# Optimization experiments

Measured on AMD Instinct MI355X. Metric: run time of the kernel, lower is better.

The kernel has to match this reference:

```python
import jax, jax.numpy as jnp
import numpy as np

DIM = 1024
HEADS = 16

def setup_inputs() -> dict:
    key = jax.random.key(0)
    k1, k2, k3, k4 = jax.random.split(key, 4)
    x = jax.random.normal(k1, (2, 2048, DIM), dtype=jnp.float32)
    # torch Linear weights are [out_features, in_features]
    w_qkv = jax.random.normal(k2, (3 * DIM, DIM), dtype=jnp.float32) * (DIM ** -0.5)
    w_out = jax.random.normal(k3, (DIM, DIM), dtype=jnp.float32) * (DIM ** -0.5)
    b_out = jax.random.normal(k4, (DIM,), dtype=jnp.float32) * 0.01
    return {"x": x, "w_qkv": w_qkv, "w_out": w_out, "b_out": b_out}

def reference(x, w_qkv, w_out, b_out):
    b, n, dim = x.shape
    h = HEADS
    d = dim // h
    scale = dim ** -0.5  # NOTE: full dim, faithful to source
    qkv = x @ w_qkv.T                       # [b, n, 3*dim]
    qkv = qkv.reshape(b, n, 3, h, d)        # split (qkv h d)
    q, k, v = (qkv[:, :, i].transpose(0, 2, 1, 3) for i in range(3))  # [b, h, n, d]
    scores = jnp.einsum('bhid,bhjd->bhij', q, k) * scale
    weights = jax.nn.softmax(scores, axis=-1)
    out = jnp.einsum('bhij,bhjd->bhid', weights, v)  # [b, h, n, d]
    out = out.transpose(0, 2, 1, 3).reshape(b, n, dim)
    return out @ w_out.T + b_out
```

## Files before the change

kernel.cpp:

```cpp
#include <hip/hip_runtime.h>

#define DIM   1024
#define HEADS 16
#define NSEQ  2048
#define BATCH 2

typedef unsigned short u16;
typedef unsigned long long u64;
typedef __attribute__((ext_vector_type(8))) short bf16x8;
typedef __attribute__((ext_vector_type(4))) float f32x4;
typedef __attribute__((ext_vector_type(16))) float f32x16;

__device__ __forceinline__ u16 f2b(float f) {
  union { float f; unsigned u; } v; v.f = f;
  unsigned r = (v.u + 0x7fffu + ((v.u >> 16) & 1u)) >> 16;
  return (u16)r;
}

__device__ __forceinline__ void g2l16(const u16* g, u16* l) {
  __builtin_amdgcn_global_load_lds(
      (const __attribute__((address_space(1))) void*)g,
      (__attribute__((address_space(3))) void*)l, 16, 0, 0);
}

__global__ void cvt_bf16(const float* __restrict__ src, u16* __restrict__ dst,
                         int n4, int sc4, float s) {
  int i = blockIdx.x * blockDim.x + threadIdx.x;
  if (i < n4) {
    float4 f = ((const float4*)src)[i];
    float m = (i < sc4) ? s : 1.0f;
    union { u16 s[4]; u64 ll; } o;
    o.s[0] = f2b(f.x * m); o.s[1] = f2b(f.y * m);
    o.s[2] = f2b(f.z * m); o.s[3] = f2b(f.w * m);
    ((u64*)dst)[i] = o.ll;
  }
}

__global__ __launch_bounds__(256, 2)
void gemm_bt(const u16* __restrict__ A, const u16* __restrict__ Bt,
             void* __restrict__ C, const float* __restrict__ bias,
             int M, int Nc, int K, int bf16_out) {
  __shared__ u16 As[128 * 64];
  __shared__ u16 Bs[128 * 64];
  const int tid  = threadIdx.x;
  const int wave = tid >> 6, lane = tid & 63;
  const int l15  = lane & 15, quad = lane >> 4;
  const int m0 = blockIdx.y * 128, n0 = blockIdx.x * 128;
  const int wm = (wave >> 1) * 64, wn = (wave & 1) * 64;
  const int rb = wave * 32;

  f32x4 acc[4][4] = {};

  for (int kt = 0; kt < K; kt += 64) {
#pragma unroll
    for (int c = 0; c < 4; ++c) {
      int r  = rb + c * 8 + (lane >> 3);
      int ck = (lane & 7) ^ (r & 7);
      g2l16(A  + (size_t)(m0 + r) * K + kt + ck * 8, &As[(rb + c * 8) * 64]);
      g2l16(Bt + (size_t)(n0 + r) * K + kt + ck * 8, &Bs[(rb + c * 8) * 64]);
    }
    __syncthreads();
#pragma unroll
    for (int ks = 0; ks < 2; ++ks) {
      bf16x8 a[4], b[4];
      int ch = ks * 4 + quad;
#pragma unroll
      for (int i = 0; i < 4; ++i) {
        int ra  = wm + i * 16 + l15;
        a[i] = *(const bf16x8*)&As[ra * 64 + ((ch ^ (ra & 7)) << 3)];
        int rb2 = wn + i * 16 + l15;
        b[i] = *(const bf16x8*)&Bs[rb2 * 64 + ((ch ^ (rb2 & 7)) << 3)];
      }
#pragma unroll
      for (int i = 0; i < 4; ++i)
#pragma unroll
        for (int j = 0; j < 4; ++j)
          acc[i][j] = __builtin_amdgcn_mfma_f32_16x16x32_bf16(a[i], b[j], acc[i][j], 0, 0, 0);
    }
    __syncthreads();
  }

#pragma unroll
  for (int i = 0; i < 4; ++i)
#pragma unroll
    for (int j = 0; j < 4; ++j) {
      int row = m0 + wm + i * 16 + quad * 4;
      int col = n0 + wn + j * 16 + l15;
#pragma unroll
      for (int r = 0; r < 4; ++r) {
        float v = acc[i][j][r];
        if (bf16_out) ((u16*)C)[(size_t)(row + r) * Nc + col] = f2b(v);
        else          ((float*)C)[(size_t)(row + r) * Nc + col] = v + bias[col];
      }
    }
}

__global__ __launch_bounds__(256, 1)
void attn(const u16* __restrict__ qkv, u16* __restrict__ outp) {
  __shared__ u16 Ks[2][128 * 64];
  __shared__ u16 Vts[2][64 * 128];
  const int tid  = threadIdx.x;
  const int wave = tid >> 6, lane = tid & 63;
  const int l31  = lane & 31, h = lane >> 5;
  const int b = blockIdx.x >> 4, hd = blockIdx.x & 15;
  const int q0 = blockIdx.y * 256;
  const u16* base = qkv + (size_t)b * NSEQ * 3072;
  const int qoff = hd * 64, koff = DIM + hd * 64, voff = 2 * DIM + hd * 64;
  const int dc = tid & 7, j0l = (tid >> 3) * 4;
  const int vchunk = (j0l >> 4) * 2 + ((j0l >> 2) & 1);
  const int vboff  = 4 * ((j0l >> 3) & 1);

  union V4 { uint4 q; u16 s[8]; };
  union PA { unsigned w[4]; bf16x8 f; };

#pragma unroll
  for (int c = 0; c < 8; ++c) {
    int bse = wave * 64 + c * 8;
    g2l16(base + (size_t)(q0 + bse + (lane >> 3)) * 3072 + qoff + (((lane & 7) ^ ((lane >> 3) & 7)) << 3),
          &Ks[bse >> 7][(bse & 127) * 64]);
  }
  __syncthreads();
  bf16x8 qf[2][4];
#pragma unroll
  for (int qg = 0; qg < 2; ++qg) {
    int qr = wave * 64 + qg * 32 + l31;
#pragma unroll
    for (int kd = 0; kd < 4; ++kd)
      qf[qg][kd] = *(const bf16x8*)&Ks[qr >> 7][(qr & 127) * 64 + (((kd * 2 + h) ^ (qr & 7)) << 3)];
  }
  __syncthreads();

  V4 vr[4];
#pragma unroll
  for (int c = 0; c < 4; ++c) {
    int bse = wave * 32 + c * 8;
    g2l16(base + (size_t)(bse + (lane >> 3)) * 3072 + koff + (((lane & 7) ^ ((lane >> 3) & 7)) << 3),
          &Ks[0][bse * 64]);
  }
#pragma unroll
  for (int e = 0; e < 4; ++e)
    vr[e].q = *(const uint4*)(base + (size_t)(j0l + e) * 3072 + voff + dc * 8);
#pragma unroll
  for (int u = 0; u < 8; ++u) {
    int d = dc * 8 + u;
    unsigned w0 = (unsigned)vr[0].s[u] | ((unsigned)vr[1].s[u] << 16);
    unsigned w1 = (unsigned)vr[2].s[u] | ((unsigned)vr[3].s[u] << 16);
    *(u64*)&Vts[0][d * 128 + ((vchunk ^ ((d + (d >> 3)) & 15)) << 3) + vboff] =
        (u64)w0 | ((u64)w1 << 32);
  }
  __syncthreads();

  float lrun[2] = {0.0f, 0.0f};
  f32x16 oacc[2][2] = {};

  for (int t = 0; t < 16; ++t) {
    const int pbuf = t & 1;
    if (t < 15) {
      const int j0n = (t + 1) * 128;
#pragma unroll
      for (int c = 0; c < 4; ++c) {
        int bse = wave * 32 + c * 8;
        g2l16(base + (size_t)(j0n + bse + (lane >> 3)) * 3072 + koff + (((lane & 7) ^ ((lane >> 3) & 7)) << 3),
              &Ks[pbuf ^ 1][bse * 64]);
      }
#pragma unroll
      for (int e = 0; e < 4; ++e)
        vr[e].q = *(const uint4*)(base + (size_t)(j0n + j0l + e) * 3072 + voff + dc * 8);
    }

    f32x16 sc[2][4] = {};
#pragma unroll
    for (int kd = 0; kd < 4; ++kd) {
      bf16x8 kb[4];
#pragma unroll
      for (int ni = 0; ni < 4; ++ni) {
        int kr = ni * 32 + l31;
        kb[ni] = *(const bf16x8*)&Ks[pbuf][kr * 64 + (((kd * 2 + h) ^ (kr & 7)) << 3)];
      }
#pragma unroll
      for (int qg = 0; qg < 2; ++qg)
#pragma unroll
        for (int ni = 0; ni < 4; ++ni)
          sc[qg][ni] = __builtin_amdgcn_mfma_f32_32x32x16_bf16(kb[ni], qf[qg][kd], sc[qg][ni], 0, 0, 0);
    }

    PA pa[2][8];
#pragma unroll
    for (int qg = 0; qg < 2; ++qg)
#pragma unroll
      for (int ni = 0; ni < 4; ++ni) {
        f32x16 p;
#pragma unroll
        for (int r = 0; r < 16; ++r) p[r] = __builtin_amdgcn_exp2f(sc[qg][ni][r]);
        float s0 = (p[0] + p[1]) + (p[2] + p[3]);
        float s1 = (p[4] + p[5]) + (p[6] + p[7]);
        float s2 = (p[8] + p[9]) + (p[10] + p[11]);
        float s3 = (p[12] + p[13]) + (p[14] + p[15]);
        lrun[qg] += (s0 + s1) + (s2 + s3);
#pragma unroll
        for (int ks2 = 0; ks2 < 2; ++ks2)
#pragma unroll
          for (int i = 0; i < 4; ++i) {
            unsigned lo = (__float_as_uint(p[8 * ks2 + 2 * i])     + 0x8000u) >> 16;
            unsigned hi = (__float_as_uint(p[8 * ks2 + 2 * i + 1]) + 0x8000u) & 0xFFFF0000u;
            pa[qg][2 * ni + ks2].w[i] = lo | hi;
          }
      }

#pragma unroll
    for (int f = 0; f < 8; ++f) {
      bf16x8 vb[2];
#pragma unroll
      for (int nd = 0; nd < 2; ++nd) {
        int d = nd * 32 + l31;
        vb[nd] = *(const bf16x8*)&Vts[pbuf][d * 128 + (((2 * f + h) ^ ((d + (d >> 3)) & 15)) << 3)];
      }
#pragma unroll
      for (int qg = 0; qg < 2; ++qg)
#pragma unroll
        for (int nd = 0; nd < 2; ++nd)
          oacc[qg][nd] = __builtin_amdgcn_mfma_f32_32x32x16_bf16(pa[qg][f].f, vb[nd], oacc[qg][nd], 0, 0, 0);
    }

    if (t < 15) {
#pragma unroll
      for (int u = 0; u < 8; ++u) {
        int d = dc * 8 + u;
        unsigned w0 = (unsigned)vr[0].s[u] | ((unsigned)vr[1].s[u] << 16);
        unsigned w1 = (unsigned)vr[2].s[u] | ((unsigned)vr[3].s[u] << 16);
        *(u64*)&Vts[pbuf ^ 1][d * 128 + ((vchunk ^ ((d + (d >> 3)) & 15)) << 3) + vboff] =
            (u64)w0 | ((u64)w1 << 32);
      }
    }
    __syncthreads();
  }

  float linv[2];
#pragma unroll
  for (int qg = 0; qg < 2; ++qg) {
    float l = lrun[qg] + __shfl_xor(lrun[qg], 32, 64);
    linv[qg] = 1.0f / l;
  }
#pragma unroll
  for (int qg = 0; qg < 2; ++qg)
#pragma unroll
    for (int r = 0; r < 16; ++r) {
      int rowloc = (r & 3) + 8 * (r >> 2) + 4 * h;
      float lb = __shfl(linv[qg], rowloc, 64);
      int row = q0 + wave * 64 + qg * 32 + rowloc;
#pragma unroll
      for (int nd = 0; nd < 2; ++nd)
        outp[((size_t)b * NSEQ + row) * DIM + hd * 64 + nd * 32 + l31] = f2b(oacc[qg][nd][r] * lb);
    }
}

extern "C" void kernel_launch(void* const* d_in, const int* in_sizes, int n_in,
                              void* d_out, int out_size, void* d_ws, size_t ws_size,
                              hipStream_t stream) {
  const float* x     = (const float*)d_in[0];
  const float* w_qkv = (const float*)d_in[1];
  const float* w_out = (const float*)d_in[2];
  const float* b_out = (const float*)d_in[3];
  float* outp = (float*)d_out;

  u16* xb    = (u16*)d_ws;
  u16* wqkvb = xb    + (size_t)4096 * 1024;
  u16* woutb = wqkvb + (size_t)3072 * 1024;
  u16* qkvb  = woutb + (size_t)1024 * 1024;
  u16* attnb = qkvb  + (size_t)4096 * 3072;

  const float C2 = 0.03125f * 1.44269504088896340736f;

  cvt_bf16<<<4096 * 1024 / 4 / 256, 256, 0, stream>>>(x,     xb,    4096 * 1024 / 4, 0, 1.0f);
  cvt_bf16<<<3072 * 1024 / 4 / 256, 256, 0, stream>>>(w_qkv, wqkvb, 3072 * 1024 / 4,
                                                      1024 * 1024 / 4, C2);
  cvt_bf16<<<1024 * 1024 / 4 / 256, 256, 0, stream>>>(w_out, woutb, 1024 * 1024 / 4, 0, 1.0f);

  gemm_bt<<<dim3(24, 32), 256, 0, stream>>>(xb, wqkvb, qkvb, nullptr, 4096, 3072, 1024, 1);
  attn<<<dim3(32, 8), 256, 0, stream>>>(qkvb, attnb);
  gemm_bt<<<dim3(8, 32), 256, 0, stream>>>(attnb, woutb, outp, b_out, 4096, 1024, 1024, 0);
}
```

Baseline: 203.7 us.

## Halve attention query tile for more blocks and use fp16 for PV product

Each attention block now handles 128 queries instead of 256, which doubles the grid to 512 blocks and raises the launch bound to two blocks per CU so there is more parallelism and occupancy. K/V tiles are now loaded twice as often per query, so reuse drops. The QKV GEMM writes the V section as fp16, and P is packed with cvt_pkrtz into fp16 so the PV MFMA runs in f16, which replaces the manual bf16 rounding and gives more mantissa precision for P.

```diff
diff --git a/kernel.cpp b/kernel.cpp
--- a/kernel.cpp
+++ b/kernel.cpp
@@ -8,6 +8,8 @@
 typedef unsigned short u16;
 typedef unsigned long long u64;
 typedef __attribute__((ext_vector_type(8))) short bf16x8;
+typedef __attribute__((ext_vector_type(8))) _Float16 f16x8;
+typedef __attribute__((ext_vector_type(2))) __fp16 pkh2;
 typedef __attribute__((ext_vector_type(4))) float f32x4;
 typedef __attribute__((ext_vector_type(16))) float f32x16;
 
@@ -15,6 +17,11 @@
   union { float f; unsigned u; } v; v.f = f;
   unsigned r = (v.u + 0x7fffu + ((v.u >> 16) & 1u)) >> 16;
   return (u16)r;
+}
+
+__device__ __forceinline__ u16 f2h(float f) {
+  _Float16 h = (_Float16)f;
+  return __builtin_bit_cast(u16, h);
 }
 
 __device__ __forceinline__ void g2l16(const u16* g, u16* l) {
@@ -39,7 +46,7 @@
 __global__ __launch_bounds__(256, 2)
 void gemm_bt(const u16* __restrict__ A, const u16* __restrict__ Bt,
              void* __restrict__ C, const float* __restrict__ bias,
-             int M, int Nc, int K, int bf16_out) {
+             int M, int Nc, int K, int mode) {
   __shared__ u16 As[128 * 64];
   __shared__ u16 Bs[128 * 64];
   const int tid  = threadIdx.x;
@@ -80,6 +87,7 @@
     __syncthreads();
   }
 
+  const int as_f16 = (mode == 2) && (n0 >= 2048);
 #pragma unroll
   for (int i = 0; i < 4; ++i)
 #pragma unroll
@@ -89,13 +97,13 @@
 #pragma unroll
       for (int r = 0; r < 4; ++r) {
         float v = acc[i][j][r];
-        if (bf16_out) ((u16*)C)[(size_t)(row + r) * Nc + col] = f2b(v);
-        else          ((float*)C)[(size_t)(row + r) * Nc + col] = v + bias[col];
-      }
-    }
-}
-
-__global__ __launch_bounds__(256, 1)
+        if (mode == 0) ((float*)C)[(size_t)(row + r) * Nc + col] = v + bias[col];
+        else ((u16*)C)[(size_t)(row + r) * Nc + col] = as_f16 ? f2h(v) : f2b(v);
+      }
+    }
+}
+
+__global__ __launch_bounds__(256, 2)
 void attn(const u16* __restrict__ qkv, u16* __restrict__ outp) {
   __shared__ u16 Ks[2][128 * 64];
   __shared__ u16 Vts[2][64 * 128];
@@ -103,7 +111,7 @@
   const int wave = tid >> 6, lane = tid & 63;
   const int l31  = lane & 31, h = lane >> 5;
   const int b = blockIdx.x >> 4, hd = blockIdx.x & 15;
-  const int q0 = blockIdx.y * 256;
+  const int q0 = blockIdx.y * 128;
   const u16* base = qkv + (size_t)b * NSEQ * 3072;
   const int qoff = hd * 64, koff = DIM + hd * 64, voff = 2 * DIM + hd * 64;
   const int dc = tid & 7, j0l = (tid >> 3) * 4;
@@ -111,22 +119,21 @@
   const int vboff  = 4 * ((j0l >> 3) & 1);
 
   union V4 { uint4 q; u16 s[8]; };
-  union PA { unsigned w[4]; bf16x8 f; };
-
-#pragma unroll
-  for (int c = 0; c < 8; ++c) {
-    int bse = wave * 64 + c * 8;
+  union PA { unsigned w[4]; f16x8 f; };
+
+#pragma unroll
+  for (int c = 0; c < 4; ++c) {
+    int bse = wave * 32 + c * 8;
     g2l16(base + (size_t)(q0 + bse + (lane >> 3)) * 3072 + qoff + (((lane & 7) ^ ((lane >> 3) & 7)) << 3),
-          &Ks[bse >> 7][(bse & 127) * 64]);
+          &Ks[0][bse * 64]);
   }
   __syncthreads();
-  bf16x8 qf[2][4];
-#pragma unroll
-  for (int qg = 0; qg < 2; ++qg) {
-    int qr = wave * 64 + qg * 32 + l31;
+  bf16x8 qf[4];
+  {
+    int qr = wave * 32 + l31;
 #pragma unroll
     for (int kd = 0; kd < 4; ++kd)
-      qf[qg][kd] = *(const bf16x8*)&Ks[qr >> 7][(qr & 127) * 64 + (((kd * 2 + h) ^ (qr & 7)) << 3)];
+      qf[kd] = *(const bf16x8*)&Ks[0][qr * 64 + (((kd * 2 + h) ^ (qr & 7)) << 3)];
   }
   __syncthreads();
 
@@ -150,8 +157,8 @@
   }
   __syncthreads();
 
-  float lrun[2] = {0.0f, 0.0f};
-  f32x16 oacc[2][2] = {};
+  float lrun = 0.0f;
+  f32x16 oacc[2] = {};
 
   for (int t = 0; t < 16; ++t) {
     const int pbuf = t & 1;
@@ -168,7 +175,7 @@
         vr[e].q = *(const uint4*)(base + (size_t)(j0n + j0l + e) * 3072 + voff + dc * 8);
     }
 
-    f32x16 sc[2][4] = {};
+    f32x16 sc[4] = {};
 #pragma unroll
     for (int kd = 0; kd < 4; ++kd) {
       bf16x8 kb[4];
@@ -178,48 +185,41 @@
         kb[ni] = *(const bf16x8*)&Ks[pbuf][kr * 64 + (((kd * 2 + h) ^ (kr & 7)) << 3)];
       }
 #pragma unroll
-      for (int qg = 0; qg < 2; ++qg)
-#pragma unroll
-        for (int ni = 0; ni < 4; ++ni)
-          sc[qg][ni] = __builtin_amdgcn_mfma_f32_32x32x16_bf16(kb[ni], qf[qg][kd], sc[qg][ni], 0, 0, 0);
-    }
-
-    PA pa[2][8];
-#pragma unroll
-    for (int qg = 0; qg < 2; ++qg)
-#pragma unroll
-      for (int ni = 0; ni < 4; ++ni) {
-        f32x16 p;
-#pragma unroll
-        for (int r = 0; r < 16; ++r) p[r] = __builtin_amdgcn_exp2f(sc[qg][ni][r]);
-        float s0 = (p[0] + p[1]) + (p[2] + p[3]);
-        float s1 = (p[4] + p[5]) + (p[6] + p[7]);
-        float s2 = (p[8] + p[9]) + (p[10] + p[11]);
-        float s3 = (p[12] + p[13]) + (p[14] + p[15]);
-        lrun[qg] += (s0 + s1) + (s2 + s3);
-#pragma unroll
-        for (int ks2 = 0; ks2 < 2; ++ks2)
-#pragma unroll
-          for (int i = 0; i < 4; ++i) {
-            unsigned lo = (__float_as_uint(p[8 * ks2 + 2 * i])     + 0x8000u) >> 16;
-            unsigned hi = (__float_as_uint(p[8 * ks2 + 2 * i + 1]) + 0x8000u) & 0xFFFF0000u;
-            pa[qg][2 * ni + ks2].w[i] = lo | hi;
-          }
-      }
+      for (int ni = 0; ni < 4; ++ni)
+        sc[ni] = __builtin_amdgcn_mfma_f32_32x32x16_bf16(kb[ni], qf[kd], sc[ni], 0, 0, 0);
+    }
+
+    PA pa[8];
+#pragma unroll
+    for (int ni = 0; ni < 4; ++ni) {
+      f32x16 p;
+#pragma unroll
+      for (int r = 0; r < 16; ++r) p[r] = __builtin_amdgcn_exp2f(sc[ni][r]);
+      float s0 = (p[0] + p[1]) + (p[2] + p[3]);
+      float s1 = (p[4] + p[5]) + (p[6] + p[7]);
+      float s2 = (p[8] + p[9]) + (p[10] + p[11]);
+      float s3 = (p[12] + p[13]) + (p[14] + p[15]);
+      lrun += (s0 + s1) + (s2 + s3);
+#pragma unroll
+      for (int ks2 = 0; ks2 < 2; ++ks2)
+#pragma unroll
+        for (int i = 0; i < 4; ++i) {
+          pkh2 t = __builtin_amdgcn_cvt_pkrtz(p[8 * ks2 + 2 * i], p[8 * ks2 + 2 * i + 1]);
+          pa[2 * ni + ks2].w[i] = __builtin_bit_cast(unsigned, t);
+        }
+    }
 
 #pragma unroll
     for (int f = 0; f < 8; ++f) {
-      bf16x8 vb[2];
+      f16x8 vb[2];
 #pragma unroll
       for (int nd = 0; nd < 2; ++nd) {
         int d = nd * 32 + l31;
-        vb[nd] = *(const bf16x8*)&Vts[pbuf][d * 128 + (((2 * f + h) ^ ((d + (d >> 3)) & 15)) << 3)];
-      }
-#pragma unroll
-      for (int qg = 0; qg < 2; ++qg)
-#pragma unroll
-        for (int nd = 0; nd < 2; ++nd)
-          oacc[qg][nd] = __builtin_amdgcn_mfma_f32_32x32x16_bf16(pa[qg][f].f, vb[nd], oacc[qg][nd], 0, 0, 0);
+        vb[nd] = *(const f16x8*)&Vts[pbuf][d * 128 + (((2 * f + h) ^ ((d + (d >> 3)) & 15)) << 3)];
+      }
+#pragma unroll
+      for (int nd = 0; nd < 2; ++nd)
+        oacc[nd] = __builtin_amdgcn_mfma_f32_32x32x16_f16(pa[f].f, vb[nd], oacc[nd], 0, 0, 0);
     }
 
     if (t < 15) {
@@ -235,23 +235,16 @@
     __syncthreads();
   }
 
-  float linv[2];
-#pragma unroll
-  for (int qg = 0; qg < 2; ++qg) {
-    float l = lrun[qg] + __shfl_xor(lrun[qg], 32, 64);
-    linv[qg] = 1.0f / l;
-  }
-#pragma unroll
-  for (int qg = 0; qg < 2; ++qg)
-#pragma unroll
-    for (int r = 0; r < 16; ++r) {
-      int rowloc = (r & 3) + 8 * (r >> 2) + 4 * h;
-      float lb = __shfl(linv[qg], rowloc, 64);
-      int row = q0 + wave * 64 + qg * 32 + rowloc;
-#pragma unroll
-      for (int nd = 0; nd < 2; ++nd)
-        outp[((size_t)b * NSEQ + row) * DIM + hd * 64 + nd * 32 + l31] = f2b(oacc[qg][nd][r] * lb);
-    }
+  float linv = 1.0f / (lrun + __shfl_xor(lrun, 32, 64));
+#pragma unroll
+  for (int r = 0; r < 16; ++r) {
+    int rowloc = (r & 3) + 8 * (r >> 2) + 4 * h;
+    float lb = __shfl(linv, rowloc, 64);
+    int row = q0 + wave * 32 + rowloc;
+#pragma unroll
+    for (int nd = 0; nd < 2; ++nd)
+      outp[((size_t)b * NSEQ + row) * DIM + hd * 64 + nd * 32 + l31] = f2b(oacc[nd][r] * lb);
+  }
 }
 
 extern "C" void kernel_launch(void* const* d_in, const int* in_sizes, int n_in,
@@ -276,7 +269,7 @@
                                                       1024 * 1024 / 4, C2);
   cvt_bf16<<<1024 * 1024 / 4 / 256, 256, 0, stream>>>(w_out, woutb, 1024 * 1024 / 4, 0, 1.0f);
 
-  gemm_bt<<<dim3(24, 32), 256, 0, stream>>>(xb, wqkvb, qkvb, nullptr, 4096, 3072, 1024, 1);
-  attn<<<dim3(32, 8), 256, 0, stream>>>(qkvb, attnb);
+  gemm_bt<<<dim3(24, 32), 256, 0, stream>>>(xb, wqkvb, qkvb, nullptr, 4096, 3072, 1024, 2);
+  attn<<<dim3(32, 16), 256, 0, stream>>>(qkvb, attnb);
   gemm_bt<<<dim3(8, 32), 256, 0, stream>>>(attnb, woutb, outp, b_out, 4096, 1024, 1024, 0);
 }
```

Result: no change. 206.9 us (+1.6%).
